# Performance work log

Hardware: AMD Instinct MI355X
Metric: run time of the kernel (lower is better)

The kernel has to match this reference:

```python
import jax, jax.numpy as jnp
import numpy as np

HEAD_SIZE = 64
NEG_INF = float('-inf')


def setup_inputs() -> dict:
    key = jax.random.key(0)
    ks = jax.random.split(key, 4)
    B, S, H, D = 8, 4096, 1024, HEAD_SIZE
    scale = 1.0 / np.sqrt(H)
    return {
        'x': jax.random.normal(ks[0], (B, S, H), dtype=jnp.float32),
        'Wq': jax.random.normal(ks[1], (H, D), dtype=jnp.float32) * scale,
        'bq': jnp.zeros((D,), dtype=jnp.float32),
        'Wk': jax.random.normal(ks[2], (H, D), dtype=jnp.float32) * scale,
        'bk': jnp.zeros((D,), dtype=jnp.float32),
        'Wv': jax.random.normal(ks[3], (H, D), dtype=jnp.float32) * scale,
        'bv': jnp.zeros((D,), dtype=jnp.float32),
    }


def reference(x, Wq, bq, Wk, bk, Wv, bv):
    # x: [B, S, H]; projections -> [B, S, D]
    B, S, H = x.shape
    q = jnp.einsum('bsh,hd->bsd', x, Wq) + bq
    k = jnp.einsum('bsh,hd->bsd', x, Wk) + bk
    v = jnp.einsum('bsh,hd->bsd', x, Wv) + bv
    # raw scores [B, S, S]
    scores = jnp.einsum('bqd,bkd->bqk', q, k)
    # causal mask applied BEFORE scaling (matches original; -inf/scale == -inf)
    causal = jnp.tril(jnp.ones((S, S), dtype=bool))
    scores = jnp.where(causal, scores, NEG_INF)
    scale = 1.0 / jnp.sqrt(jnp.asarray(q.shape[-1], dtype=scores.dtype))
    attn = jax.nn.softmax(scores * scale, axis=-1)
    # dropout = 0.0 (eval) -> identity
    return jnp.einsum('bqk,bkd->bqd', attn, v)
```

## Files before the change

### kernel.cpp

```cpp
#include <hip/hip_runtime.h>
#include <hip/hip_bf16.h>
#include <math.h>

#define SEQ 4096
#define HID 1024
#define DH  64
#define NB  8
#define QSCALE 0.18033688011112042f

typedef unsigned short ushort_t;
typedef unsigned int   uint_t;
typedef __attribute__((ext_vector_type(8)))  short  bf16x8;
typedef __attribute__((ext_vector_type(4)))  float  f32x4;
typedef __attribute__((ext_vector_type(16))) float  f32x16;
typedef __attribute__((ext_vector_type(4)))  uint_t u32x4;
typedef __attribute__((ext_vector_type(2)))  uint_t u32x2;

static __device__ __forceinline__ ushort_t f2bf(float f) {
    __hip_bfloat16 h = __float2bfloat16(f);
    return *reinterpret_cast<ushort_t*>(&h);
}
static __device__ __forceinline__ ushort_t f2bf_fast(float f) {
    uint_t u = __float_as_uint(f);
    return (ushort_t)((u + 0x8000u) >> 16);
}
static __device__ __forceinline__ uint_t bfpair(float lo, float hi) {
    return (uint_t)f2bf_fast(lo) | ((uint_t)f2bf_fast(hi) << 16);
}

static __device__ __forceinline__ void gld_lds16(const void* g, void* s) {
    __builtin_amdgcn_global_load_lds(
        (const __attribute__((address_space(1))) void*)g,
        (__attribute__((address_space(3))) void*)s, 16, 0, 0);
}

__global__ __launch_bounds__(256) void prep_w(
    const float* __restrict__ Wq, const float* __restrict__ Wk,
    const float* __restrict__ Wv, ushort_t* __restrict__ wts)
{
    __shared__ ushort_t tr[64][72];
    const int bx   = blockIdx.x;
    const int mmat = bx >> 4;
    const int kt   = bx & 15;
    const float* W  = (mmat == 0) ? Wq : (mmat == 1) ? Wk : Wv;
    const float  sc = (mmat == 0) ? QSCALE : 1.0f;

    const int t  = threadIdx.x;
    const int kr = t >> 2, kc = (t & 3) * 16;
    const float* src = W + (size_t)(kt * 64 + kr) * DH + kc;
    float4 a0 = *(const float4*)(src);
    float4 a1 = *(const float4*)(src + 4);
    float4 a2 = *(const float4*)(src + 8);
    float4 a3 = *(const float4*)(src + 12);
    float vv[16] = {a0.x,a0.y,a0.z,a0.w, a1.x,a1.y,a1.z,a1.w,
                    a2.x,a2.y,a2.z,a2.w, a3.x,a3.y,a3.z,a3.w};
    #pragma unroll
    for (int i = 0; i < 16; ++i) tr[kr][kc + i] = f2bf(vv[i] * sc);
    __syncthreads();

    const int cl = t >> 2, jc = (t & 3) * 16;
    const int c  = mmat * 64 + cl;
    ushort_t* dst = wts + kt * 12288 + c * 64;
    #pragma unroll
    for (int jj = 0; jj < 16; ++jj) {
        int j = jc + jj;
        dst[((j >> 3) ^ (cl & 7)) * 8 + (j & 7)] = tr[j][cl];
    }
}

__global__ __launch_bounds__(256) void qkv_proj(
    const float* __restrict__ x, const ushort_t* __restrict__ wts,
    const float* __restrict__ bq, const float* __restrict__ bk,
    const float* __restrict__ bv,
    ushort_t* __restrict__ qimg, ushort_t* __restrict__ kimg,
    ushort_t* __restrict__ vimg)
{
    extern __shared__ char dynls[];

    const int t  = threadIdx.x;
    const int w  = t >> 6, l = t & 63, lw = l & 31, hs = l >> 5;
    const int row0 = blockIdx.x * 128;
    const int row  = row0 + w * 32 + lw;

    f32x16 acc[6];
    #pragma unroll
    for (int i = 0; i < 6; ++i)
        for (int r = 0; r < 16; ++r) acc[i][r] = 0.f;

    const char* wbase = (const char*)wts;
    const int   wlo   = w * 1024 + l * 16;
    const float* xrow = x + (size_t)row * HID + hs * 8;

    auto STAGEW = [&](int ss, int tile) {
        char* bdst = dynls + ss * 24576 + w * 1024;
        const char* bsrc = wbase + (size_t)tile * 24576 + wlo;
        #pragma unroll
        for (int i = 0; i < 6; ++i)
            gld_lds16(bsrc + i * 4096, bdst + i * 4096);
    };

    float4 Xc[4][2], Xn[4][2];

    STAGEW(0, 0);
    #pragma unroll
    for (int ks = 0; ks < 4; ++ks) {
        Xc[ks][0] = *(const float4*)(xrow + ks * 16);
        Xc[ks][1] = *(const float4*)(xrow + ks * 16 + 4);
    }
    STAGEW(1, 1);

    int cs = 0;
    for (int kt = 0; kt < 16; ++kt) {
        if (kt < 15) asm volatile("s_waitcnt vmcnt(6)" ::: "memory");
        else         asm volatile("s_waitcnt vmcnt(0)" ::: "memory");
        __builtin_amdgcn_s_barrier();
        asm volatile("" ::: "memory");

        if (kt < 15) {
            const float* xn = xrow + (kt + 1) * 64;
            #pragma unroll
            for (int ks = 0; ks < 4; ++ks) {
                Xn[ks][0] = *(const float4*)(xn + ks * 16);
                Xn[ks][1] = *(const float4*)(xn + ks * 16 + 4);
            }
        }
        if (kt < 14) {
            const int sd = (cs == 0) ? 2 : cs - 1;
            STAGEW(sd, kt + 2);
        }

        bf16x8 af[4];
        #pragma unroll
        for (int ks = 0; ks < 4; ++ks) {
            u32x4 p;
            p.x = bfpair(Xc[ks][0].x, Xc[ks][0].y);
            p.y = bfpair(Xc[ks][0].z, Xc[ks][0].w);
            p.z = bfpair(Xc[ks][1].x, Xc[ks][1].y);
            p.w = bfpair(Xc[ks][1].z, Xc[ks][1].w);
            af[ks] = *(bf16x8*)&p;
        }
        const ushort_t* bwS = (const ushort_t*)(dynls + cs * 24576);
        #pragma unroll
        for (int ct = 0; ct < 6; ++ct) {
            const ushort_t* bp = bwS + (ct * 32 + lw) * 64;
            #pragma unroll
            for (int ks = 0; ks < 4; ++ks) {
                bf16x8 bf = *(const bf16x8*)(bp + (((ks * 2 + hs) ^ (lw & 7)) * 8));
                acc[ct] = __builtin_amdgcn_mfma_f32_32x32x16_bf16(af[ks], bf, acc[ct], 0, 0, 0);
            }
        }
        #pragma unroll
        for (int ks = 0; ks < 4; ++ks) { Xc[ks][0] = Xn[ks][0]; Xc[ks][1] = Xn[ks][1]; }
        cs = (cs == 2) ? 0 : cs + 1;
    }

    const int rowbase = row0 + w * 32;
    #pragma unroll
    for (int ct = 0; ct < 6; ++ct) {
        const int mmat = ct >> 1;
        const int cc   = ((ct & 1) << 5) | lw;
        const float* bpv = (mmat == 0) ? bq : (mmat == 1) ? bk : bv;
        const float bias = bpv[cc] * (mmat == 0 ? QSCALE : 1.0f);
        #pragma unroll
        for (int r = 0; r < 16; ++r) {
            const int s = rowbase + (r & 3) + 8 * (r >> 2) + 4 * hs;
            const ushort_t v = f2bf_fast(acc[ct][r] + bias);
            if (mmat == 0)
                qimg[(size_t)s * 64 + cc] = v;
            else if (mmat == 1)
                kimg[(size_t)(s >> 6) * 4096 + (s & 63) * 64 +
                     ((cc >> 3) ^ (s & 7)) * 8 + (cc & 7)] = v;
            else
                vimg[(size_t)(s >> 6) * 4096 + (size_t)cc * 64 +
                     (((s & 63) >> 3) ^ (cc & 7)) * 8 + (s & 7)] = v;
        }
    }
}

__global__ __launch_bounds__(256) void attn(
    const ushort_t* __restrict__ qimg, const ushort_t* __restrict__ kimg,
    const ushort_t* __restrict__ vimg,
    float* __restrict__ Opart, float* __restrict__ Lpart)
{
    __shared__ ushort_t kvs[3][8192];
    float* const oscp  = (float*)&kvs[0][0];
    float* const lredp = (float*)&kvs[1][0];

    const int t  = threadIdx.x;
    const int w  = t >> 6, l = t & 63, lw = l & 31, hs = l >> 5;
    const int qh = w & 1;
    const int kh = w >> 1;
    const int bx   = blockIdx.x;
    const int half = bx & 1;
    const int u    = bx >> 1;
    const int qt   = 63 - (u >> 3);
    const int b    = u & 7;
    const int q0   = qt * 64;
    const int n    = qt + 1, hn = n >> 1;
    const int t0   = half ? hn : 0;
    const int t1   = half ? n : hn;
    const int qq   = q0 + qh * 32 + lw;

    bf16x8 qf[4];
    {
        const ushort_t* qp = qimg + (size_t)(b * SEQ + qq) * 64 + hs * 8;
        #pragma unroll
        for (int ks = 0; ks < 4; ++ks) qf[ks] = *(const bf16x8*)(qp + ks * 16);
    }

    f32x16 o0, o1;
    #pragma unroll
    for (int r = 0; r < 16; ++r) { o0[r] = 0.f; o1[r] = 0.f; }
    float lpart = 0.f;

    const char* kbase = (const char*)kimg + (size_t)b * 524288;
    const char* vbase = (const char*)vimg + (size_t)b * 524288;
    const int wo = w * 1024;
    const int lo = l * 16;

    auto STAGE = [&](int ss, int tt) {
        const char* ks = kbase + (size_t)tt * 8192;
        const char* vs = vbase + (size_t)tt * 8192;
        char* lk = (char*)&kvs[ss][0];
        gld_lds16(ks + wo + lo,        lk + wo);
        gld_lds16(ks + wo + lo + 4096, lk + wo + 4096);
        gld_lds16(vs + wo + lo,        lk + wo + 8192);
        gld_lds16(vs + wo + lo + 4096, lk + wo + 12288);
    };

    if (t0     < t1) STAGE(0, t0);
    if (t0 + 1 < t1) STAGE(1, t0 + 1);

    int cur = 0;
    for (int kt = t0; kt < t1; ++kt) {
        if (kt + 1 < t1) asm volatile("s_waitcnt vmcnt(4)" ::: "memory");
        else             asm volatile("s_waitcnt vmcnt(0)" ::: "memory");
        __builtin_amdgcn_s_barrier();
        asm volatile("" ::: "memory");
        if (kt + 2 < t1) {
            const int sd = (cur == 0) ? 2 : cur - 1;
            STAGE(sd, kt + 2);
        }

        const ushort_t* kb   = &kvs[cur][0];
        const int       krow = kh * 32 + lw;
        const ushort_t* krb  = kb + krow * 64;
        f32x16 s;
        #pragma unroll
        for (int r = 0; r < 16; ++r) s[r] = 0.f;
        #pragma unroll
        for (int ks = 0; ks < 4; ++ks) {
            bf16x8 kf = *(const bf16x8*)(krb + (((ks * 2 + hs) ^ (krow & 7)) * 8));
            s = __builtin_amdgcn_mfma_f32_32x32x16_bf16(kf, qf[ks], s, 0, 0, 0);
        }

        float p[16];
        if (kt == qt) {
            #pragma unroll
            for (int r = 0; r < 16; ++r) {
                const int kvg = kt * 64 + kh * 32 + (r & 3) + 8 * (r >> 2) + 4 * hs;
                p[r] = (kvg > qq) ? 0.f : __builtin_amdgcn_exp2f(s[r]);
            }
        } else {
            #pragma unroll
            for (int r = 0; r < 16; ++r) p[r] = __builtin_amdgcn_exp2f(s[r]);
        }
        {
            float s0 = (p[0] + p[1])  + (p[2] + p[3]);
            float s1 = (p[4] + p[5])  + (p[6] + p[7]);
            float s2 = (p[8] + p[9])  + (p[10] + p[11]);
            float s3 = (p[12] + p[13]) + (p[14] + p[15]);
            lpart += (s0 + s1) + (s2 + s3);
        }

        const ushort_t* vb = &kvs[cur][4096];
        #pragma unroll
        for (int ks2 = 0; ks2 < 2; ++ks2) {
            uint_t a0 = bfpair(p[ks2*8 + 0], p[ks2*8 + 1]);
            uint_t b0 = bfpair(p[ks2*8 + 4], p[ks2*8 + 5]);
            uint_t a1 = bfpair(p[ks2*8 + 2], p[ks2*8 + 3]);
            uint_t b1 = bfpair(p[ks2*8 + 6], p[ks2*8 + 7]);
            asm("v_permlane32_swap_b32 %0, %1" : "+v"(a0), "+v"(b0));
            asm("v_permlane32_swap_b32 %0, %1" : "+v"(a1), "+v"(b1));
            u32x4 pw = { a0, a1, b0, b1 };
            bf16x8 paf = *(bf16x8*)&pw;
            const int sl8 = kh * 4 + ks2 * 2 + hs;
            {
                const int vr0 = lw;
                bf16x8 vf0 = *(const bf16x8*)(vb + vr0 * 64 + ((sl8 ^ (vr0 & 7)) * 8));
                o0 = __builtin_amdgcn_mfma_f32_32x32x16_bf16(paf, vf0, o0, 0, 0, 0);
                const int vr1 = 32 + lw;
                bf16x8 vf1 = *(const bf16x8*)(vb + vr1 * 64 + ((sl8 ^ (vr1 & 7)) * 8));
                o1 = __builtin_amdgcn_mfma_f32_32x32x16_bf16(paf, vf1, o1, 0, 0, 0);
            }
        }
        cur = (cur == 2) ? 0 : cur + 1;
    }
    __syncthreads();

    if (kh == 1) {
        const int lbase = (qh * 64 + l) * 32;
        #pragma unroll
        for (int i = 0; i < 4; ++i) {
            f32x4 v = { o0[4*i], o0[4*i+1], o0[4*i+2], o0[4*i+3] };
            *(f32x4*)&oscp[lbase + ((i ^ (l & 7)) * 4)] = v;
        }
        #pragma unroll
        for (int i = 0; i < 4; ++i) {
            f32x4 v = { o1[4*i], o1[4*i+1], o1[4*i+2], o1[4*i+3] };
            *(f32x4*)&oscp[lbase + (((i + 4) ^ (l & 7)) * 4)] = v;
        }
        float lsum = lpart + __shfl_xor(lpart, 32);
        if (hs == 0) lredp[qh * 32 + lw] = lsum;
    }
    __syncthreads();
    if (kh == 0) {
        const int lbase = (qh * 64 + l) * 32;
        #pragma unroll
        for (int i = 0; i < 4; ++i) {
            f32x4 v = *(const f32x4*)&oscp[lbase + ((i ^ (l & 7)) * 4)];
            o0[4*i] += v.x; o0[4*i+1] += v.y; o0[4*i+2] += v.z; o0[4*i+3] += v.w;
        }
        #pragma unroll
        for (int i = 0; i < 4; ++i) {
            f32x4 v = *(const f32x4*)&oscp[lbase + (((i + 4) ^ (l & 7)) * 4)];
            o1[4*i] += v.x; o1[4*i+1] += v.y; o1[4*i+2] += v.z; o1[4*i+3] += v.w;
        }
        const float lt = (lpart + __shfl_xor(lpart, 32)) + lredp[qh * 32 + lw];

        const int m = b * 64 + qt;
        float* Op = Opart + ((size_t)half * 512 + m) * 4096;
        #pragma unroll
        for (int r = 0; r < 16; ++r) {
            const int qrow = qh * 32 + (r & 3) + 8 * (r >> 2) + 4 * hs;
            Op[qrow * 64 + lw]      = o0[r];
            Op[qrow * 64 + 32 + lw] = o1[r];
        }
        if (hs == 0)
            Lpart[((size_t)half * 512 + m) * 64 + qh * 32 + lw] = lt;
    }
}

__global__ __launch_bounds__(256) void merge_o(
    const float* __restrict__ Opart, const float* __restrict__ Lpart,
    float* __restrict__ outg)
{
    const int m = blockIdx.x;
    const int b = m >> 6, qt = m & 63;
    const int t = threadIdx.x;
    const int row = t >> 2, c = (t & 3) * 16;

    const float* A = Opart + (size_t)m * 4096 + row * 64 + c;
    const float* B = Opart + (size_t)(512 + m) * 4096 + row * 64 + c;
    const float la = Lpart[(size_t)m * 64 + row];
    const float lb = Lpart[(size_t)(512 + m) * 64 + row];
    const float inv = 1.0f / (la + lb);
    float* dst = outg + ((size_t)b * SEQ + qt * 64 + row) * 64 + c;
    #pragma unroll
    for (int j = 0; j < 4; ++j) {
        float4 va = *(const float4*)(A + j * 4);
        float4 vb = *(const float4*)(B + j * 4);
        float4 vo = { (va.x + vb.x) * inv, (va.y + vb.y) * inv,
                      (va.z + vb.z) * inv, (va.w + vb.w) * inv };
        *(float4*)(dst + j * 4) = vo;
    }
}

extern "C" void kernel_launch(void* const* d_in, const int* in_sizes, int n_in,
                              void* d_out, int out_size, void* d_ws, size_t ws_size,
                              hipStream_t stream) {
    const float* x  = (const float*)d_in[0];
    const float* Wq = (const float*)d_in[1];
    const float* bq = (const float*)d_in[2];
    const float* Wk = (const float*)d_in[3];
    const float* bk = (const float*)d_in[4];
    const float* Wv = (const float*)d_in[5];
    const float* bv = (const float*)d_in[6];
    float* out = (float*)d_out;

    const size_t per = (size_t)NB * SEQ * DH;
    ushort_t* q   = (ushort_t*)d_ws;
    ushort_t* k   = q + per;
    ushort_t* v   = k + per;
    ushort_t* wts = v + per;
    float* Opart  = (float*)((char*)d_ws + (size_t)(16u << 20));
    float* Lpart  = (float*)((char*)d_ws + (size_t)(40u << 20));

    prep_w  <<<dim3(48),   256, 0,     stream>>>(Wq, Wk, Wv, wts);
    qkv_proj<<<dim3(256),  256, 73728, stream>>>(x, wts, bq, bk, bv, q, k, v);
    attn    <<<dim3(1024), 256, 0,     stream>>>(q, k, v, Opart, Lpart);
    merge_o <<<dim3(512),  256, 0,     stream>>>(Opart, Lpart, out);
}
```

Before: 261.3 us.

## Split QKV projection tiles across waves and use double-buffered static LDS

The QKV projection block now covers 64 rows instead of 128. The four waves split as two row halves by two column halves, so each wave holds 3 accumulator tiles instead of 6, and the grid doubles to 512 blocks. The weight staging drops from a triple-buffered dynamic LDS ring to a static double buffer with a barrier after compute. This targets more parallelism and occupancy in the memory-bound x read. In exchange each block re-reads the full weight tile for half as many rows, and the extra barrier per k-step reduces overlap.

Result: no change. 261.8 us (+0.2%).

```diff
diff --git a/kernel.cpp b/kernel.cpp
--- a/kernel.cpp
+++ b/kernel.cpp
@@ -75,16 +75,18 @@
     ushort_t* __restrict__ qimg, ushort_t* __restrict__ kimg,
     ushort_t* __restrict__ vimg)
 {
-    extern __shared__ char dynls[];
+    __shared__ ushort_t bw[2][12288];
 
     const int t  = threadIdx.x;
     const int w  = t >> 6, l = t & 63, lw = l & 31, hs = l >> 5;
-    const int row0 = blockIdx.x * 128;
-    const int row  = row0 + w * 32 + lw;
-
-    f32x16 acc[6];
-    #pragma unroll
-    for (int i = 0; i < 6; ++i)
+    const int rh = w & 1;
+    const int ch = w >> 1;
+    const int row0 = blockIdx.x * 64;
+    const int row  = row0 + rh * 32 + lw;
+
+    f32x16 acc[3];
+    #pragma unroll
+    for (int i = 0; i < 3; ++i)
         for (int r = 0; r < 16; ++r) acc[i][r] = 0.f;
 
     const char* wbase = (const char*)wts;
@@ -92,7 +94,7 @@
     const float* xrow = x + (size_t)row * HID + hs * 8;
 
     auto STAGEW = [&](int ss, int tile) {
-        char* bdst = dynls + ss * 24576 + w * 1024;
+        char* bdst = (char*)&bw[ss][0] + w * 1024;
         const char* bsrc = wbase + (size_t)tile * 24576 + wlo;
         #pragma unroll
         for (int i = 0; i < 6; ++i)
@@ -107,16 +109,11 @@
         Xc[ks][0] = *(const float4*)(xrow + ks * 16);
         Xc[ks][1] = *(const float4*)(xrow + ks * 16 + 4);
     }
-    STAGEW(1, 1);
-
-    int cs = 0;
+
     for (int kt = 0; kt < 16; ++kt) {
-        if (kt < 15) asm volatile("s_waitcnt vmcnt(6)" ::: "memory");
-        else         asm volatile("s_waitcnt vmcnt(0)" ::: "memory");
-        __builtin_amdgcn_s_barrier();
-        asm volatile("" ::: "memory");
-
+        const int buf = kt & 1;
         if (kt < 15) {
+            STAGEW(buf ^ 1, kt + 1);
             const float* xn = xrow + (kt + 1) * 64;
             #pragma unroll
             for (int ks = 0; ks < 4; ++ks) {
@@ -124,10 +121,10 @@
                 Xn[ks][1] = *(const float4*)(xn + ks * 16 + 4);
             }
         }
-        if (kt < 14) {
-            const int sd = (cs == 0) ? 2 : cs - 1;
-            STAGEW(sd, kt + 2);
-        }
+        if (kt < 15) asm volatile("s_waitcnt vmcnt(14)" ::: "memory");
+        else         asm volatile("s_waitcnt vmcnt(0)"  ::: "memory");
+        __builtin_amdgcn_s_barrier();
+        asm volatile("" ::: "memory");
 
         bf16x8 af[4];
         #pragma unroll
@@ -139,26 +136,29 @@
             p.w = bfpair(Xc[ks][1].z, Xc[ks][1].w);
             af[ks] = *(bf16x8*)&p;
         }
-        const ushort_t* bwS = (const ushort_t*)(dynls + cs * 24576);
-        #pragma unroll
-        for (int ct = 0; ct < 6; ++ct) {
-            const ushort_t* bp = bwS + (ct * 32 + lw) * 64;
+        const ushort_t* bwS = &bw[buf][0];
+        #pragma unroll
+        for (int ct = 0; ct < 3; ++ct) {
+            const int c32 = ch * 3 + ct;
+            const ushort_t* bp = bwS + (c32 * 32 + lw) * 64;
             #pragma unroll
             for (int ks = 0; ks < 4; ++ks) {
                 bf16x8 bf = *(const bf16x8*)(bp + (((ks * 2 + hs) ^ (lw & 7)) * 8));
                 acc[ct] = __builtin_amdgcn_mfma_f32_32x32x16_bf16(af[ks], bf, acc[ct], 0, 0, 0);
             }
         }
+        asm volatile("" ::: "memory");
+        __builtin_amdgcn_s_barrier();
         #pragma unroll
         for (int ks = 0; ks < 4; ++ks) { Xc[ks][0] = Xn[ks][0]; Xc[ks][1] = Xn[ks][1]; }
-        cs = (cs == 2) ? 0 : cs + 1;
-    }
-
-    const int rowbase = row0 + w * 32;
-    #pragma unroll
-    for (int ct = 0; ct < 6; ++ct) {
-        const int mmat = ct >> 1;
-        const int cc   = ((ct & 1) << 5) | lw;
+    }
+
+    const int rowbase = row0 + rh * 32;
+    #pragma unroll
+    for (int ct = 0; ct < 3; ++ct) {
+        const int c32  = ch * 3 + ct;
+        const int mmat = c32 >> 1;
+        const int cc   = ((c32 & 1) << 5) | lw;
         const float* bpv = (mmat == 0) ? bq : (mmat == 1) ? bk : bv;
         const float bias = bpv[cc] * (mmat == 0 ? QSCALE : 1.0f);
         #pragma unroll
@@ -386,8 +386,8 @@
     float* Opart  = (float*)((char*)d_ws + (size_t)(16u << 20));
     float* Lpart  = (float*)((char*)d_ws + (size_t)(40u << 20));
 
-    prep_w  <<<dim3(48),   256, 0,     stream>>>(Wq, Wk, Wv, wts);
-    qkv_proj<<<dim3(256),  256, 73728, stream>>>(x, wts, bq, bk, bv, q, k, v);
-    attn    <<<dim3(1024), 256, 0,     stream>>>(q, k, v, Opart, Lpart);
-    merge_o <<<dim3(512),  256, 0,     stream>>>(Opart, Lpart, out);
-}
+    prep_w  <<<dim3(48),   256, 0, stream>>>(Wq, Wk, Wv, wts);
+    qkv_proj<<<dim3(512),  256, 0, stream>>>(x, wts, bq, bk, bv, q, k, v);
+    attn    <<<dim3(1024), 256, 0, stream>>>(q, k, v, Opart, Lpart);
+    merge_o <<<dim3(512),  256, 0, stream>>>(Opart, Lpart, out);
+}
```
